# Kernel optimization log

Hardware: AMD Instinct MI355X
Metric: run time of the kernel (lower is better)

The kernel has to match this reference:

```python
import jax, jax.numpy as jnp
import numpy as np

NX, NY, D, K = 20000, 50000, 64, 8
NUM_BATCHES = 2


def _knn_np(px, py, bx, by, k):
    # Batched exact kNN via chunked squared-distance + argpartition (mirrors torch_cluster.knn under no_grad).
    pp = (px * px).sum(1)
    idx = np.empty((py.shape[0], k), np.int32)
    chunk = 4096
    for s in range(0, py.shape[0], chunk):
        q = py[s:s + chunk]
        d = (q * q).sum(1)[:, None] + pp[None, :] - 2.0 * (q @ px.T)
        d = np.where(by[s:s + chunk, None] == bx[None, :], d, np.inf)
        idx[s:s + chunk] = np.argpartition(d, k, axis=1)[:, :k].astype(np.int32)
    return idx


def setup_inputs() -> dict:
    rng = np.random.default_rng(0)
    pos_x = (rng.random((NX, 3)) * 10.0).astype(np.float32)
    pos_y = (rng.random((NY, 3)) * 10.0).astype(np.float32)
    bx = np.repeat(np.arange(NUM_BATCHES), NX // NUM_BATCHES).astype(np.int32)
    by = np.repeat(np.arange(NUM_BATCHES), NY // NUM_BATCHES).astype(np.int32)
    x_idx = _knn_np(pos_x, pos_y, bx, by, K).reshape(-1)            # [NY*K]
    y_idx = np.repeat(np.arange(NY, dtype=np.int32), K)             # [NY*K]

    key = jax.random.key(0)
    ks = jax.random.split(key, 6)

    def lin(k, fi, fo):
        return jax.random.normal(k, (fi, fo), jnp.float32) / np.sqrt(fi).astype(np.float32)

    return {
        "x": jax.random.normal(ks[0], (NX, D), jnp.float32),
        "pos_x": jnp.asarray(pos_x),
        "pos_y": jnp.asarray(pos_y),
        "x_idx": jnp.asarray(x_idx),
        "y_idx": jnp.asarray(y_idx),
        # ResnetBlockFC 1: size_in=D+3, size_h=D, size_out=D (shortcut linear, no bias)
        "W0a": lin(ks[1], D + 3, D), "b0a": jnp.zeros((D,), jnp.float32),
        "W1a": lin(ks[2], D, D),     "b1a": jnp.zeros((D,), jnp.float32),
        "Wsa": lin(ks[3], D + 3, D),
        # ResnetBlockFC 2: size_in=size_h=size_out=D (identity shortcut)
        "W0b": lin(ks[4], D, D),     "b0b": jnp.zeros((D,), jnp.float32),
        "W1b": lin(ks[5], D, D),     "b1b": jnp.zeros((D,), jnp.float32),
    }


def reference(x, pos_x, pos_y, x_idx, y_idx, W0a, b0a, W1a, b1a, Wsa, W0b, b0b, W1b, b1b):
    # gather + positional diff (diff computed under no_grad in the original)
    diff = jax.lax.stop_gradient(pos_x[x_idx] - pos_y[y_idx])        # [E, 3]
    h = jnp.concatenate([x[x_idx], diff], axis=1)                    # [E, D+3]
    # ResnetBlockFC 1: out = shortcut(h) + fc1(relu(fc0(relu(h))))
    net = jax.nn.relu(h) @ W0a + b0a
    dx = jax.nn.relu(net) @ W1a + b1a
    h = h @ Wsa + dx                                                 # [E, D]
    # ResnetBlockFC 2 (identity shortcut)
    net = jax.nn.relu(h) @ W0b + b0b
    h = h + jax.nn.relu(net) @ W1b + b1b                             # [E, D]
    # scatter-max back to query points (every query has exactly K edges)
    out = jax.ops.segment_max(h, y_idx, num_segments=NY)             # [NY, D]
    return out
```

## Files before the change

### kernel.cpp

```cpp
#include <hip/hip_runtime.h>


typedef _Float16 f16x8 __attribute__((ext_vector_type(8)));
typedef _Float16 f16x4 __attribute__((ext_vector_type(4)));
typedef float    f32x4 __attribute__((ext_vector_type(4)));

constexpr int NX      = 20000;
constexpr int NROWS   = 50000 * 8;
constexpr int NTILES  = NROWS / 16;
constexpr int NFRAG   = 48;
constexpr int TSTRIDE = 72;
constexpr int BW      = 12;
constexpr int BLOCK   = 64 * BW;

__global__ void prep_x(const float* __restrict__ x, _Float16* __restrict__ x16) {
    const int i = blockIdx.x * blockDim.x + threadIdx.x;
    if (i < NX * 16) {
        float4 v = ((const float4*)x)[i];
        f16x4 o = {(_Float16)v.x, (_Float16)v.y, (_Float16)v.z, (_Float16)v.w};
        *(f16x4*)(x16 + (size_t)i * 4) = o;
    }
}

static __device__ __forceinline__ void xpose_relu(const f32x4* acc, const float* bb,
                                                  _Float16* tbuf, int q, int n0,
                                                  f16x8* af) {
    __threadfence_block();
#pragma unroll
    for (int t = 0; t < 4; ++t)
#pragma unroll
        for (int r = 0; r < 4; ++r) {
            float v = acc[t][r] + bb[t];
            tbuf[(q * 4 + r) * TSTRIDE + t * 16 + n0] = (_Float16)(v > 0.0f ? v : 0.0f);
        }
    __threadfence_block();
#pragma unroll
    for (int s = 0; s < 2; ++s)
        af[s] = *(const f16x8*)&tbuf[n0 * TSTRIDE + s * 32 + q * 8];
}

__global__ __launch_bounds__(BLOCK, 6)
void pointnet_fused(const _Float16* __restrict__ x16,
                    const float* __restrict__ pos_x,
                    const float* __restrict__ pos_y,
                    const int*   __restrict__ x_idx,
                    const float* __restrict__ W0a, const float* __restrict__ b0a,
                    const float* __restrict__ W1a, const float* __restrict__ b1a,
                    const float* __restrict__ Wsa,
                    const float* __restrict__ W0b, const float* __restrict__ b0b,
                    const float* __restrict__ W1b, const float* __restrict__ b1b,
                    float* __restrict__ out)
{
    __shared__ __align__(16) _Float16 bfrag[NFRAG * 64 * 8];
    __shared__ __align__(16) _Float16 trans[BW][16 * TSTRIDE];
    __shared__ float bias_lds[4 * 64];

    const int tid = threadIdx.x;

    for (int p = tid; p < NFRAG * 64; p += BLOCK) {
        const int f = p >> 6;
        const int l = p & 63;
        const float* W; int krows, fl;
        if (f < 12)      { W = W0a; krows = 67; fl = f; }
        else if (f < 20) { W = W1a; krows = 64; fl = f - 12; }
        else if (f < 32) { W = Wsa; krows = 67; fl = f - 20; }
        else if (f < 40) { W = W0b; krows = 64; fl = f - 32; }
        else             { W = W1b; krows = 64; fl = f - 40; }
        const int s = fl >> 2, t = fl & 3;
        const int n = t * 16 + (l & 15);
        const int kbase = s * 32 + (l >> 4) * 8;
        f16x8 v;
#pragma unroll
        for (int j = 0; j < 8; ++j) {
            const int k = kbase + j;
            v[j] = (_Float16)((k < krows) ? W[k * 64 + n] : 0.0f);
        }
        *(f16x8*)&bfrag[p * 8] = v;
    }
    if (tid < 256) {
        const int L = tid >> 6, i = tid & 63;
        const float* b = (L == 0) ? b0a : (L == 1) ? b1a : (L == 2) ? b0b : b1b;
        bias_lds[tid] = b[i];
    }
    __syncthreads();

    const int lane = tid & 63;
    const int wv   = tid >> 6;
    const int n0   = lane & 15;
    const int q    = lane >> 4;

    _Float16* tbuf = trans[wv];
    const int gwave  = blockIdx.x * BW + wv;
    const int nwaves = gridDim.x * BW;

    for (int tile = gwave; tile < NTILES; tile += nwaves) {
        const int row = tile * 16 + n0;
        const int xi  = x_idx[row];
        const _Float16* xp = x16 + (long)xi * 64 + q * 8;
        f16x8 hn[3];
        hn[0] = *(const f16x8*)(xp);
        hn[1] = *(const f16x8*)(xp + 32);
        {
            f16x8 z = {};
            hn[2] = z;
            if (q == 0) {
                const int yi = row >> 3;
#pragma unroll
                for (int j = 0; j < 3; ++j)
                    hn[2][j] = (_Float16)(pos_x[xi * 3 + j] - pos_y[yi * 3 + j]);
            }
        }

        f32x4 A2[4];
#pragma unroll
        for (int t = 0; t < 4; ++t)
            A2[t] = (f32x4){0.f, 0.f, 0.f, 0.f};
#pragma unroll
        for (int s = 0; s < 3; ++s)
#pragma unroll
            for (int t = 0; t < 4; ++t) {
                f16x8 b = *(const f16x8*)&bfrag[((20 + s * 4 + t) * 64 + lane) * 8];
                A2[t] = __builtin_amdgcn_mfma_f32_16x16x32_f16(hn[s], b, A2[t], 0, 0, 0);
            }

#pragma unroll
        for (int s = 0; s < 3; ++s)
#pragma unroll
            for (int j = 0; j < 8; ++j) {
                _Float16 v = hn[s][j];
                hn[s][j] = v > (_Float16)0 ? v : (_Float16)0;
            }

        f32x4 A1[4];
#pragma unroll
        for (int t = 0; t < 4; ++t)
            A1[t] = (f32x4){0.f, 0.f, 0.f, 0.f};
#pragma unroll
        for (int s = 0; s < 3; ++s)
#pragma unroll
            for (int t = 0; t < 4; ++t) {
                f16x8 b = *(const f16x8*)&bfrag[((s * 4 + t) * 64 + lane) * 8];
                A1[t] = __builtin_amdgcn_mfma_f32_16x16x32_f16(hn[s], b, A1[t], 0, 0, 0);
            }

        float bb[4];
#pragma unroll
        for (int t = 0; t < 4; ++t) bb[t] = bias_lds[0 * 64 + t * 16 + n0];
        f16x8 a2f[2];
        xpose_relu(A1, bb, tbuf, q, n0, a2f);
#pragma unroll
        for (int s = 0; s < 2; ++s)
#pragma unroll
            for (int t = 0; t < 4; ++t) {
                f16x8 b = *(const f16x8*)&bfrag[((12 + s * 4 + t) * 64 + lane) * 8];
                A2[t] = __builtin_amdgcn_mfma_f32_16x16x32_f16(a2f[s], b, A2[t], 0, 0, 0);
            }

#pragma unroll
        for (int t = 0; t < 4; ++t) bb[t] = bias_lds[1 * 64 + t * 16 + n0];
#pragma unroll
        for (int t = 0; t < 4; ++t)
#pragma unroll
            for (int r = 0; r < 4; ++r)
                A2[t][r] += bb[t];
        const float bz[4] = {0.f, 0.f, 0.f, 0.f};
        f16x8 a4f[2];
        xpose_relu(A2, bz, tbuf, q, n0, a4f);

        f32x4 A3[4];
#pragma unroll
        for (int t = 0; t < 4; ++t)
            A3[t] = (f32x4){0.f, 0.f, 0.f, 0.f};
#pragma unroll
        for (int s = 0; s < 2; ++s)
#pragma unroll
            for (int t = 0; t < 4; ++t) {
                f16x8 b = *(const f16x8*)&bfrag[((32 + s * 4 + t) * 64 + lane) * 8];
                A3[t] = __builtin_amdgcn_mfma_f32_16x16x32_f16(a4f[s], b, A3[t], 0, 0, 0);
            }

#pragma unroll
        for (int t = 0; t < 4; ++t) bb[t] = bias_lds[2 * 64 + t * 16 + n0];
        f16x8 a5f[2];
        xpose_relu(A3, bb, tbuf, q, n0, a5f);

#pragma unroll
        for (int t = 0; t < 4; ++t) bb[t] = bias_lds[3 * 64 + t * 16 + n0];
#pragma unroll
        for (int t = 0; t < 4; ++t)
#pragma unroll
            for (int r = 0; r < 4; ++r)
                A2[t][r] += bb[t];
#pragma unroll
        for (int s = 0; s < 2; ++s)
#pragma unroll
            for (int t = 0; t < 4; ++t) {
                f16x8 b = *(const f16x8*)&bfrag[((40 + s * 4 + t) * 64 + lane) * 8];
                A2[t] = __builtin_amdgcn_mfma_f32_16x16x32_f16(a5f[s], b, A2[t], 0, 0, 0);
            }

#pragma unroll
        for (int t = 0; t < 4; ++t) {
            float pm = fmaxf(fmaxf(A2[t][0], A2[t][1]),
                             fmaxf(A2[t][2], A2[t][3]));
            pm = fmaxf(pm, __shfl_xor(pm, 16, 64));
            if ((q & 1) == 0) {
                const int y = tile * 2 + (q >> 1);
                out[(long)y * 64 + t * 16 + n0] = pm;
            }
        }
    }
}

extern "C" void kernel_launch(void* const* d_in, const int* in_sizes, int n_in,
                              void* d_out, int out_size, void* d_ws, size_t ws_size,
                              hipStream_t stream) {
    (void)in_sizes; (void)n_in; (void)ws_size; (void)out_size;
    _Float16* x16 = (_Float16*)d_ws;

    prep_x<<<(NX * 16 + 255) / 256, 256, 0, stream>>>((const float*)d_in[0], x16);

    pointnet_fused<<<512, BLOCK, 0, stream>>>(
        x16,
        (const float*)d_in[1],
        (const float*)d_in[2],
        (const int*)  d_in[3],
        (const float*)d_in[5],  (const float*)d_in[6],
        (const float*)d_in[7],  (const float*)d_in[8],
        (const float*)d_in[9],
        (const float*)d_in[10], (const float*)d_in[11],
        (const float*)d_in[12], (const float*)d_in[13],
        (float*)d_out);
}
```

Baseline: 126.5 us.

## Compute transposed MFMA products to chain layers in registers with biases folded in

Swaps the MFMA operand order so each layer's output accumulator is already in the B-fragment layout for the next layer. This removes the per-layer LDS transpose round trips and their fences. Biases move into the weight fragments as an extra K row, multiplied by a constant-one input or fragment, so the bias-add loops disappear at the cost of extra MFMAs. The segment max now goes through an fp16 LDS staging buffer plus shuffles and vectorized stores, which rounds the final output to half precision. Waves per block and the occupancy hint also change.

```diff
diff --git a/kernel.cpp b/kernel.cpp
--- a/kernel.cpp
+++ b/kernel.cpp
@@ -5,13 +5,13 @@
 typedef _Float16 f16x4 __attribute__((ext_vector_type(4)));
 typedef float    f32x4 __attribute__((ext_vector_type(4)));
 
-constexpr int NX      = 20000;
-constexpr int NROWS   = 50000 * 8;
-constexpr int NTILES  = NROWS / 16;
-constexpr int NFRAG   = 48;
-constexpr int TSTRIDE = 72;
-constexpr int BW      = 12;
-constexpr int BLOCK   = 64 * BW;
+constexpr int NX     = 20000;
+constexpr int NROWS  = 50000 * 8;
+constexpr int NTILES = NROWS / 16;
+constexpr int NFRAG  = 60;
+constexpr int BW     = 8;
+constexpr int BLOCK  = 64 * BW;
+constexpr int TS2    = 72;
 
 __global__ void prep_x(const float* __restrict__ x, _Float16* __restrict__ x16) {
     const int i = blockIdx.x * blockDim.x + threadIdx.x;
@@ -22,24 +22,20 @@
     }
 }
 
-static __device__ __forceinline__ void xpose_relu(const f32x4* acc, const float* bb,
-                                                  _Float16* tbuf, int q, int n0,
-                                                  f16x8* af) {
-    __threadfence_block();
-#pragma unroll
-    for (int t = 0; t < 4; ++t)
-#pragma unroll
-        for (int r = 0; r < 4; ++r) {
-            float v = acc[t][r] + bb[t];
-            tbuf[(q * 4 + r) * TSTRIDE + t * 16 + n0] = (_Float16)(v > 0.0f ? v : 0.0f);
-        }
-    __threadfence_block();
-#pragma unroll
-    for (int s = 0; s < 2; ++s)
-        af[s] = *(const f16x8*)&tbuf[n0 * TSTRIDE + s * 32 + q * 8];
-}
-
-__global__ __launch_bounds__(BLOCK, 6)
+static __device__ __forceinline__ void pack_relu(const f32x4* A, f16x8* bf) {
+#pragma unroll
+    for (int s = 0; s < 2; ++s) {
+        f16x8 r;
+#pragma unroll
+        for (int e = 0; e < 8; ++e) {
+            float v = A[2 * s + (e >> 2)][e & 3];
+            r[e] = (_Float16)(v > 0.0f ? v : 0.0f);
+        }
+        bf[s] = r;
+    }
+}
+
+__global__ __launch_bounds__(BLOCK, 4)
 void pointnet_fused(const _Float16* __restrict__ x16,
                     const float* __restrict__ pos_x,
                     const float* __restrict__ pos_y,
@@ -52,35 +48,35 @@
                     float* __restrict__ out)
 {
     __shared__ __align__(16) _Float16 bfrag[NFRAG * 64 * 8];
-    __shared__ __align__(16) _Float16 trans[BW][16 * TSTRIDE];
-    __shared__ float bias_lds[4 * 64];
+    __shared__ __align__(16) _Float16 ebuf[BW][16 * TS2];
 
     const int tid = threadIdx.x;
 
     for (int p = tid; p < NFRAG * 64; p += BLOCK) {
-        const int f = p >> 6;
-        const int l = p & 63;
-        const float* W; int krows, fl;
-        if (f < 12)      { W = W0a; krows = 67; fl = f; }
-        else if (f < 20) { W = W1a; krows = 64; fl = f - 12; }
-        else if (f < 32) { W = Wsa; krows = 67; fl = f - 20; }
-        else if (f < 40) { W = W0b; krows = 64; fl = f - 32; }
-        else             { W = W1b; krows = 64; fl = f - 40; }
-        const int s = fl >> 2, t = fl & 3;
-        const int n = t * 16 + (l & 15);
-        const int kbase = s * 32 + (l >> 4) * 8;
+        const int f = p >> 6, l = p & 63;
+        const int q = l >> 4, n0 = l & 15;
+        const int grp = f / 12, fl = f % 12, s = fl >> 2, t = fl & 3;
+        const int col = t * 16 + n0;
         f16x8 v;
 #pragma unroll
         for (int j = 0; j < 8; ++j) {
-            const int k = kbase + j;
-            v[j] = (_Float16)((k < krows) ? W[k * 64 + n] : 0.0f);
+            const int k = 32 * s + 8 * q + j;
+            float val = 0.0f;
+            if (grp == 0)      val = (k < 67) ? W0a[k * 64 + col] : (k == 67 ? b0a[col] : 0.0f);
+            else if (grp == 1) val = (k < 67) ? Wsa[k * 64 + col] : 0.0f;
+            else {
+                const float* W  = (grp == 2) ? W1a : (grp == 3) ? W0b : W1b;
+                const float* bb = (grp == 2) ? b1a : (grp == 3) ? b0b : b1b;
+                if (s < 2) {
+                    const int row = 32 * s + 16 * (j >> 2) + 4 * q + (j & 3);
+                    val = W[row * 64 + col];
+                } else {
+                    val = (q == 0 && j == 0) ? bb[col] : 0.0f;
+                }
+            }
+            v[j] = (_Float16)val;
         }
         *(f16x8*)&bfrag[p * 8] = v;
-    }
-    if (tid < 256) {
-        const int L = tid >> 6, i = tid & 63;
-        const float* b = (L == 0) ? b0a : (L == 1) ? b1a : (L == 2) ? b0b : b1b;
-        bias_lds[tid] = b[i];
     }
     __syncthreads();
 
@@ -89,9 +85,19 @@
     const int n0   = lane & 15;
     const int q    = lane >> 4;
 
-    _Float16* tbuf = trans[wv];
+    _Float16* eb = ebuf[wv];
+
+    f16x8 bfr = {};
+    if (q == 0) bfr[0] = (_Float16)1.0f;
+
+    const int ey  = (lane >> 3) & 1;
+    const int efg = lane & 7;
+    const int esb = lane >> 4;
+
     const int gwave  = blockIdx.x * BW + wv;
     const int nwaves = gridDim.x * BW;
+
+#define WFRAG(fid) (*(const f16x8*)&bfrag[(((fid) * 64) + lane) * 8])
 
     for (int tile = gwave; tile < NTILES; tile += nwaves) {
         const int row = tile * 16 + n0;
@@ -108,20 +114,18 @@
 #pragma unroll
                 for (int j = 0; j < 3; ++j)
                     hn[2][j] = (_Float16)(pos_x[xi * 3 + j] - pos_y[yi * 3 + j]);
+                hn[2][3] = (_Float16)1.0f;
             }
         }
 
         f32x4 A2[4];
 #pragma unroll
-        for (int t = 0; t < 4; ++t)
-            A2[t] = (f32x4){0.f, 0.f, 0.f, 0.f};
+        for (int t = 0; t < 4; ++t) A2[t] = (f32x4){0.f, 0.f, 0.f, 0.f};
 #pragma unroll
         for (int s = 0; s < 3; ++s)
 #pragma unroll
-            for (int t = 0; t < 4; ++t) {
-                f16x8 b = *(const f16x8*)&bfrag[((20 + s * 4 + t) * 64 + lane) * 8];
-                A2[t] = __builtin_amdgcn_mfma_f32_16x16x32_f16(hn[s], b, A2[t], 0, 0, 0);
-            }
+            for (int t = 0; t < 4; ++t)
+                A2[t] = __builtin_amdgcn_mfma_f32_16x16x32_f16(WFRAG(12 + s * 4 + t), hn[s], A2[t], 0, 0, 0);
 
 #pragma unroll
         for (int s = 0; s < 3; ++s)
@@ -130,86 +134,76 @@
                 _Float16 v = hn[s][j];
                 hn[s][j] = v > (_Float16)0 ? v : (_Float16)0;
             }
-
         f32x4 A1[4];
 #pragma unroll
-        for (int t = 0; t < 4; ++t)
-            A1[t] = (f32x4){0.f, 0.f, 0.f, 0.f};
+        for (int t = 0; t < 4; ++t) A1[t] = (f32x4){0.f, 0.f, 0.f, 0.f};
 #pragma unroll
         for (int s = 0; s < 3; ++s)
 #pragma unroll
-            for (int t = 0; t < 4; ++t) {
-                f16x8 b = *(const f16x8*)&bfrag[((s * 4 + t) * 64 + lane) * 8];
-                A1[t] = __builtin_amdgcn_mfma_f32_16x16x32_f16(hn[s], b, A1[t], 0, 0, 0);
-            }
-
-        float bb[4];
-#pragma unroll
-        for (int t = 0; t < 4; ++t) bb[t] = bias_lds[0 * 64 + t * 16 + n0];
-        f16x8 a2f[2];
-        xpose_relu(A1, bb, tbuf, q, n0, a2f);
-#pragma unroll
-        for (int s = 0; s < 2; ++s)
-#pragma unroll
-            for (int t = 0; t < 4; ++t) {
-                f16x8 b = *(const f16x8*)&bfrag[((12 + s * 4 + t) * 64 + lane) * 8];
-                A2[t] = __builtin_amdgcn_mfma_f32_16x16x32_f16(a2f[s], b, A2[t], 0, 0, 0);
-            }
-
-#pragma unroll
-        for (int t = 0; t < 4; ++t) bb[t] = bias_lds[1 * 64 + t * 16 + n0];
-#pragma unroll
-        for (int t = 0; t < 4; ++t)
-#pragma unroll
-            for (int r = 0; r < 4; ++r)
-                A2[t][r] += bb[t];
-        const float bz[4] = {0.f, 0.f, 0.f, 0.f};
-        f16x8 a4f[2];
-        xpose_relu(A2, bz, tbuf, q, n0, a4f);
-
+            for (int t = 0; t < 4; ++t)
+                A1[t] = __builtin_amdgcn_mfma_f32_16x16x32_f16(WFRAG(s * 4 + t), hn[s], A1[t], 0, 0, 0);
+
+        f16x8 bf[2];
+        pack_relu(A1, bf);
+#pragma unroll
+        for (int t = 0; t < 4; ++t) {
+            A2[t] = __builtin_amdgcn_mfma_f32_16x16x32_f16(WFRAG(24 + 0 * 4 + t), bf[0], A2[t], 0, 0, 0);
+            A2[t] = __builtin_amdgcn_mfma_f32_16x16x32_f16(WFRAG(24 + 1 * 4 + t), bf[1], A2[t], 0, 0, 0);
+            A2[t] = __builtin_amdgcn_mfma_f32_16x16x32_f16(WFRAG(24 + 2 * 4 + t), bfr,   A2[t], 0, 0, 0);
+        }
+
+        pack_relu(A2, bf);
         f32x4 A3[4];
 #pragma unroll
-        for (int t = 0; t < 4; ++t)
-            A3[t] = (f32x4){0.f, 0.f, 0.f, 0.f};
-#pragma unroll
-        for (int s = 0; s < 2; ++s)
-#pragma unroll
-            for (int t = 0; t < 4; ++t) {
-                f16x8 b = *(const f16x8*)&bfrag[((32 + s * 4 + t) * 64 + lane) * 8];
-                A3[t] = __builtin_amdgcn_mfma_f32_16x16x32_f16(a4f[s], b, A3[t], 0, 0, 0);
-            }
-
-#pragma unroll
-        for (int t = 0; t < 4; ++t) bb[t] = bias_lds[2 * 64 + t * 16 + n0];
-        f16x8 a5f[2];
-        xpose_relu(A3, bb, tbuf, q, n0, a5f);
-
-#pragma unroll
-        for (int t = 0; t < 4; ++t) bb[t] = bias_lds[3 * 64 + t * 16 + n0];
-#pragma unroll
-        for (int t = 0; t < 4; ++t)
-#pragma unroll
-            for (int r = 0; r < 4; ++r)
-                A2[t][r] += bb[t];
-#pragma unroll
-        for (int s = 0; s < 2; ++s)
-#pragma unroll
-            for (int t = 0; t < 4; ++t) {
-                f16x8 b = *(const f16x8*)&bfrag[((40 + s * 4 + t) * 64 + lane) * 8];
-                A2[t] = __builtin_amdgcn_mfma_f32_16x16x32_f16(a5f[s], b, A2[t], 0, 0, 0);
-            }
-
-#pragma unroll
-        for (int t = 0; t < 4; ++t) {
-            float pm = fmaxf(fmaxf(A2[t][0], A2[t][1]),
-                             fmaxf(A2[t][2], A2[t][3]));
-            pm = fmaxf(pm, __shfl_xor(pm, 16, 64));
-            if ((q & 1) == 0) {
-                const int y = tile * 2 + (q >> 1);
-                out[(long)y * 64 + t * 16 + n0] = pm;
-            }
-        }
-    }
+        for (int t = 0; t < 4; ++t) A3[t] = (f32x4){0.f, 0.f, 0.f, 0.f};
+#pragma unroll
+        for (int t = 0; t < 4; ++t) {
+            A3[t] = __builtin_amdgcn_mfma_f32_16x16x32_f16(WFRAG(36 + 0 * 4 + t), bf[0], A3[t], 0, 0, 0);
+            A3[t] = __builtin_amdgcn_mfma_f32_16x16x32_f16(WFRAG(36 + 1 * 4 + t), bf[1], A3[t], 0, 0, 0);
+            A3[t] = __builtin_amdgcn_mfma_f32_16x16x32_f16(WFRAG(36 + 2 * 4 + t), bfr,   A3[t], 0, 0, 0);
+        }
+
+        pack_relu(A3, bf);
+#pragma unroll
+        for (int t = 0; t < 4; ++t) {
+            A2[t] = __builtin_amdgcn_mfma_f32_16x16x32_f16(WFRAG(48 + 0 * 4 + t), bf[0], A2[t], 0, 0, 0);
+            A2[t] = __builtin_amdgcn_mfma_f32_16x16x32_f16(WFRAG(48 + 1 * 4 + t), bf[1], A2[t], 0, 0, 0);
+            A2[t] = __builtin_amdgcn_mfma_f32_16x16x32_f16(WFRAG(48 + 2 * 4 + t), bfr,   A2[t], 0, 0, 0);
+        }
+
+        __threadfence_block();
+#pragma unroll
+        for (int t = 0; t < 4; ++t) {
+            f16x4 w;
+#pragma unroll
+            for (int r = 0; r < 4; ++r) w[r] = (_Float16)A2[t][r];
+            *(f16x4*)&eb[n0 * TS2 + t * 16 + q * 4] = w;
+        }
+        __threadfence_block();
+
+        const int dr0 = ey * 8 + esb * 2;
+        f16x8 ra = *(const f16x8*)&eb[dr0 * TS2 + efg * 8];
+        f16x8 rb = *(const f16x8*)&eb[(dr0 + 1) * TS2 + efg * 8];
+#pragma unroll
+        for (int e = 0; e < 8; ++e) ra[e] = ra[e] > rb[e] ? ra[e] : rb[e];
+#pragma unroll
+        for (int st = 0; st < 2; ++st) {
+            union { f16x8 h; int i[4]; } u, v2;
+            u.h = ra;
+#pragma unroll
+            for (int d = 0; d < 4; ++d) v2.i[d] = __shfl_xor(u.i[d], st == 0 ? 16 : 32, 64);
+#pragma unroll
+            for (int e = 0; e < 8; ++e) ra[e] = ra[e] > v2.h[e] ? ra[e] : v2.h[e];
+        }
+        if (esb == 0) {
+            float4 f0 = {(float)ra[0], (float)ra[1], (float)ra[2], (float)ra[3]};
+            float4 f1 = {(float)ra[4], (float)ra[5], (float)ra[6], (float)ra[7]};
+            float* op = out + (long)(tile * 2 + ey) * 64 + efg * 8;
+            *(float4*)op = f0;
+            *(float4*)(op + 4) = f1;
+        }
+    }
+#undef WFRAG
 }
 
 extern "C" void kernel_launch(void* const* d_in, const int* in_sizes, int n_in,
```

Measured after the change: 121.5 us. 3.9% less time.
